# Optimization experiments

Hardware: AMD Instinct MI355X
Metric: run time of the kernel (lower is better)

## Reference

```python
import jax, jax.numpy as jnp
import numpy as np

N = 100000
E = 3200000
D = 128
H = 128
BN_EPS = 1e-5


def setup_inputs() -> dict:
    key = jax.random.key(0)
    ks = jax.random.split(key, 8)
    x = jax.random.normal(ks[0], (N, D), dtype=jnp.float32)
    edge_index = jax.random.randint(ks[1], (2, E), 0, N, dtype=jnp.int64)
    edge_attr = jax.random.normal(ks[2], (E, 1), dtype=jnp.float32)
    # MLP params (Linear stores weight [out,in]; we keep [in,out] for x @ W)
    W1 = jax.random.normal(ks[3], (D, H), dtype=jnp.float32) / np.sqrt(D)
    b1 = jnp.zeros((H,), dtype=jnp.float32)
    W2 = jax.random.normal(ks[4], (H, H), dtype=jnp.float32) / np.sqrt(H)
    b2 = jnp.zeros((H,), dtype=jnp.float32)
    gamma = jnp.ones((H,), dtype=jnp.float32)
    beta = jnp.zeros((H,), dtype=jnp.float32)
    return {"x": x, "edge_index": edge_index, "edge_attr": edge_attr,
            "W1": W1, "b1": b1, "W2": W2, "b2": b2,
            "gamma": gamma, "beta": beta}


def reference(x, edge_index, edge_attr, W1, b1, W2, b2, gamma, beta):
    src, dst = edge_index[0], edge_index[1]
    # GIN aggregation: (1 + eps) * x_i + sum_{j->i} x_j, eps = 0
    agg = jax.ops.segment_sum(x[src], dst, num_segments=N)  # [N, D]
    h = x + agg
    # 2-layer MLP
    h = jax.nn.relu(h @ W1 + b1)
    h = h @ W2 + b2
    # outer ReLU
    h = jax.nn.relu(h)
    # BatchNorm1d (training mode: batch stats, biased variance)
    mean = jnp.mean(h, axis=0)
    var = jnp.mean(jnp.square(h - mean), axis=0)
    h = (h - mean) * jax.lax.rsqrt(var + BN_EPS) * gamma + beta
    return h
```

## Files before the change

### kernel.cpp

```cpp
#include <hip/hip_runtime.h>

#define N_NODES 100000
#define DIM 128
#define NBUCK 391
#define CAP 12288
#define PT_TILE 8192
#define PT_THR 512

typedef unsigned int u32;
typedef unsigned short u16;
typedef __attribute__((ext_vector_type(8))) short bf16x8;
typedef __attribute__((ext_vector_type(4))) float f32x4;

__device__ __forceinline__ float bf16_to_f(u16 v) {
  return __uint_as_float(((u32)v) << 16);
}
__device__ __forceinline__ u16 f_to_bf16(float f) {
  u32 b = __float_as_uint(f);
  b += 0x7fff + ((b >> 16) & 1);
  return (u16)(b >> 16);
}
__device__ __forceinline__ float blo(u32 q) { return __uint_as_float(q << 16); }
__device__ __forceinline__ float bhi(u32 q) {
  return __uint_as_float(q & 0xffff0000u);
}
__device__ __forceinline__ u32 packbf(float lo, float hi) {
  return ((u32)f_to_bf16(hi) << 16) | (u32)f_to_bf16(lo);
}

__global__ __launch_bounds__(256) void prep_kernel(
    const float* __restrict__ W1, u16* __restrict__ Wt1,
    const float* __restrict__ W2, u16* __restrict__ Wt2,
    const int* __restrict__ ei, int* __restrict__ bcnt, int E_) {
  int blk = blockIdx.x;
  if (blk < 64) {
    int id = blk * 256 + threadIdx.x;
    Wt1[id] = f_to_bf16(W1[(id & 127) * DIM + (id >> 7)]);
  } else if (blk < 128) {
    int id = (blk - 64) * 256 + threadIdx.x;
    Wt2[id] = f_to_bf16(W2[(id & 127) * DIM + (id >> 7)]);
  } else {
    __shared__ int lc[NBUCK];
    for (int i = threadIdx.x; i < NBUCK; i += 256) lc[i] = 0;
    __syncthreads();
    const int* dst = ei + E_;
    int G = 512 * 256;
    int g = (blk - 128) * 256 + threadIdx.x;
    int n4 = E_ >> 2;
    const int4* d4 = (const int4*)dst;
    for (int i = g; i < n4; i += G) {
      int4 v = d4[i];
      atomicAdd(&lc[((u32)v.x) >> 8], 1);
      atomicAdd(&lc[((u32)v.y) >> 8], 1);
      atomicAdd(&lc[((u32)v.z) >> 8], 1);
      atomicAdd(&lc[((u32)v.w) >> 8], 1);
    }
    for (int e = (n4 << 2) + g; e < E_; e += G)
      atomicAdd(&lc[((u32)dst[e]) >> 8], 1);
    __syncthreads();
    for (int i = threadIdx.x; i < NBUCK; i += 256)
      if (lc[i]) atomicAdd(&bcnt[i], lc[i]);
  }
}

__global__ void bscan_kernel(const int* __restrict__ bcnt,
                             int* __restrict__ boffs, int* __restrict__ gcur) {
  __shared__ int s[256];
  int t = threadIdx.x;
  int v0 = (2 * t < NBUCK) ? bcnt[2 * t] : 0;
  int v1 = (2 * t + 1 < NBUCK) ? bcnt[2 * t + 1] : 0;
  int ts = v0 + v1;
  s[t] = ts;
  __syncthreads();
  for (int o = 1; o < 256; o <<= 1) {
    int u = (t >= o) ? s[t - o] : 0;
    __syncthreads();
    s[t] += u;
    __syncthreads();
  }
  int excl = s[t] - ts;
  if (2 * t <= NBUCK) boffs[2 * t] = excl;
  if (2 * t + 1 <= NBUCK) boffs[2 * t + 1] = excl + v0;
  if (2 * t < NBUCK) gcur[2 * t] = excl;
  if (2 * t + 1 < NBUCK) gcur[2 * t + 1] = excl + v0;
}

__global__ __launch_bounds__(PT_THR) void part_cvt_kernel(
    const int* __restrict__ ei, int* __restrict__ gcur,
    u32* __restrict__ packed, int E_, const float* __restrict__ x,
    u16* __restrict__ xb) {
  __shared__ u32 keys[PT_TILE];
  __shared__ u16 bid[PT_TILE];
  __shared__ int lh[NBUCK];
  __shared__ int lpos[NBUCK];
  __shared__ int gpos[NBUCK];
  __shared__ int ss[PT_THR];
  const int nPart = (E_ + PT_TILE - 1) / PT_TILE;
  const int t = threadIdx.x;

  if (blockIdx.x >= nPart) {
    int cb = blockIdx.x - nPart;
    int total = N_NODES * DIM / 4;
    int stride = 1024 * PT_THR;
    for (int i = cb * PT_THR + t; i < total; i += stride) {
      float4 v = reinterpret_cast<const float4*>(x)[i];
      ushort4 o;
      o.x = f_to_bf16(v.x);
      o.y = f_to_bf16(v.y);
      o.z = f_to_bf16(v.z);
      o.w = f_to_bf16(v.w);
      reinterpret_cast<ushort4*>(xb)[i] = o;
    }
    return;
  }

  const int base = blockIdx.x * PT_TILE;
  const int cnt = min(PT_TILE, E_ - base);

  for (int i = t; i < NBUCK; i += PT_THR) lh[i] = 0;
  __syncthreads();

  u32 pk[16];
  int bb[16];
#pragma unroll
  for (int k = 0; k < 16; ++k) {
    int e = base + k * PT_THR + t;
    if (k * PT_THR + t < cnt) {
      int src = ei[e];
      u32 dst = (u32)ei[E_ + e];
      bb[k] = (int)(dst >> 8);
      pk[k] = (u32)src | ((dst & 255u) << 17);
      atomicAdd(&lh[bb[k]], 1);
    } else {
      bb[k] = -1;
    }
  }
  __syncthreads();

  int v = (t < NBUCK) ? lh[t] : 0;
  ss[t] = v;
  __syncthreads();
  for (int o = 1; o < PT_THR; o <<= 1) {
    int u = (t >= o) ? ss[t - o] : 0;
    __syncthreads();
    ss[t] += u;
    __syncthreads();
  }
  if (t < NBUCK) {
    lpos[t] = ss[t] - v;
    if (v > 0) gpos[t] = atomicAdd(&gcur[t], v);
  }
  __syncthreads();

#pragma unroll
  for (int k = 0; k < 16; ++k) {
    if (bb[k] >= 0) {
      int p = atomicAdd(&lpos[bb[k]], 1);
      keys[p] = pk[k];
      bid[p] = (u16)bb[k];
    }
  }
  __syncthreads();

  for (int i = t; i < cnt; i += PT_THR) {
    int b = bid[i];
    int startb = lpos[b] - lh[b];
    packed[gpos[b] + (i - startb)] = keys[i];
  }
}

__global__ __launch_bounds__(256) void bsort_kernel(u32* __restrict__ packed,
                                                    const int* __restrict__ boffs,
                                                    int* __restrict__ offs,
                                                    int E_) {
  __shared__ u32 sorted_[CAP];
  __shared__ int hist[256], cur[256], ss[256];
  const int b = blockIdx.x, t = threadIdx.x;
  int base = boffs[b];
  int cnt = boffs[b + 1] - base;
  if (cnt > CAP) cnt = CAP;
  hist[t] = 0;
  __syncthreads();
  for (int i = t; i < cnt; i += 256) atomicAdd(&hist[packed[base + i] >> 17], 1);
  __syncthreads();
  int hv = hist[t];
  ss[t] = hv;
  __syncthreads();
  for (int o = 1; o < 256; o <<= 1) {
    int u = (t >= o) ? ss[t - o] : 0;
    __syncthreads();
    ss[t] += u;
    __syncthreads();
  }
  int excl = ss[t] - hv;
  cur[t] = excl;
  __syncthreads();
  for (int i = t; i < cnt; i += 256) {
    u32 v = packed[base + i];
    int p = atomicAdd(&cur[v >> 17], 1);
    sorted_[p] = v & 0x1FFFFu;
  }
  __syncthreads();
  for (int i = t; i < cnt; i += 256) packed[base + i] = sorted_[i];
  int node = b * 256 + t;
  if (node < N_NODES) offs[node] = base + excl;
  if (b == 0 && t == 0) offs[N_NODES] = E_;
}

__global__ __launch_bounds__(256) void gather_bf16_kernel(
    const uint4* __restrict__ xb4, const int* __restrict__ offs,
    const int* __restrict__ csr, uint4* __restrict__ hb4) {
  int n = blockIdx.x * 4 + (threadIdx.x >> 6);
  int lane = threadIdx.x & 63;
  int g = lane >> 4;
  int l = lane & 15;
  int beg = offs[n], end = offs[n + 1];
  float a0 = 0.f, a1 = 0.f, a2 = 0.f, a3 = 0.f;
  float a4 = 0.f, a5 = 0.f, a6 = 0.f, a7 = 0.f;
  if (g == 0) {
    uint4 q = xb4[(size_t)n * 16 + l];
    a0 = blo(q.x); a1 = bhi(q.x);
    a2 = blo(q.y); a3 = bhi(q.y);
    a4 = blo(q.z); a5 = bhi(q.z);
    a6 = blo(q.w); a7 = bhi(q.w);
  }
  int j = beg + g;
  for (; j + 12 < end; j += 16) {
    int s0 = csr[j], s1 = csr[j + 4], s2 = csr[j + 8], s3 = csr[j + 12];
    uint4 q0 = xb4[(size_t)s0 * 16 + l];
    uint4 q1 = xb4[(size_t)s1 * 16 + l];
    uint4 q2 = xb4[(size_t)s2 * 16 + l];
    uint4 q3 = xb4[(size_t)s3 * 16 + l];
    a0 += blo(q0.x); a1 += bhi(q0.x);
    a2 += blo(q0.y); a3 += bhi(q0.y);
    a4 += blo(q0.z); a5 += bhi(q0.z);
    a6 += blo(q0.w); a7 += bhi(q0.w);
    a0 += blo(q1.x); a1 += bhi(q1.x);
    a2 += blo(q1.y); a3 += bhi(q1.y);
    a4 += blo(q1.z); a5 += bhi(q1.z);
    a6 += blo(q1.w); a7 += bhi(q1.w);
    a0 += blo(q2.x); a1 += bhi(q2.x);
    a2 += blo(q2.y); a3 += bhi(q2.y);
    a4 += blo(q2.z); a5 += bhi(q2.z);
    a6 += blo(q2.w); a7 += bhi(q2.w);
    a0 += blo(q3.x); a1 += bhi(q3.x);
    a2 += blo(q3.y); a3 += bhi(q3.y);
    a4 += blo(q3.z); a5 += bhi(q3.z);
    a6 += blo(q3.w); a7 += bhi(q3.w);
  }
  for (; j < end; j += 4) {
    uint4 q = xb4[(size_t)csr[j] * 16 + l];
    a0 += blo(q.x); a1 += bhi(q.x);
    a2 += blo(q.y); a3 += bhi(q.y);
    a4 += blo(q.z); a5 += bhi(q.z);
    a6 += blo(q.w); a7 += bhi(q.w);
  }
  a0 += __shfl_xor(a0, 16); a1 += __shfl_xor(a1, 16);
  a2 += __shfl_xor(a2, 16); a3 += __shfl_xor(a3, 16);
  a4 += __shfl_xor(a4, 16); a5 += __shfl_xor(a5, 16);
  a6 += __shfl_xor(a6, 16); a7 += __shfl_xor(a7, 16);
  a0 += __shfl_xor(a0, 32); a1 += __shfl_xor(a1, 32);
  a2 += __shfl_xor(a2, 32); a3 += __shfl_xor(a3, 32);
  a4 += __shfl_xor(a4, 32); a5 += __shfl_xor(a5, 32);
  a6 += __shfl_xor(a6, 32); a7 += __shfl_xor(a7, 32);
  if (g == 0) {
    uint4 o;
    o.x = packbf(a0, a1);
    o.y = packbf(a2, a3);
    o.z = packbf(a4, a5);
    o.w = packbf(a6, a7);
    hb4[(size_t)n * 16 + l] = o;
  }
}

__global__ __launch_bounds__(256) void mlp_mfma_kernel(
    u16* __restrict__ hb, const u16* __restrict__ Wt1,
    const u16* __restrict__ Wt2, const float* __restrict__ b1,
    const float* __restrict__ b2, float* __restrict__ pstats) {
  __shared__ u16 sH1[4][16 * DIM];
  __shared__ float sS[4][128], sQ[4][128];
  const int tid = threadIdx.x;
  const int wv = tid >> 6;
  const int lane = tid & 63;
  const int lr = lane & 15;
  const int lq = lane >> 4;
  const int row0 = blockIdx.x * 64 + wv * 16;

  bf16x8 a[4];
  {
    int r = row0 + lr;
    if (r > N_NODES - 1) r = N_NODES - 1;
#pragma unroll
    for (int ks = 0; ks < 4; ++ks)
      a[ks] = *reinterpret_cast<const bf16x8*>(hb + (size_t)r * DIM + ks * 32 +
                                               lq * 8);
  }
  f32x4 acc[8];
#pragma unroll
  for (int ct = 0; ct < 8; ++ct) {
    f32x4 c = {0.f, 0.f, 0.f, 0.f};
#pragma unroll
    for (int ks = 0; ks < 4; ++ks) {
      bf16x8 b = *reinterpret_cast<const bf16x8*>(
          Wt1 + (ct * 16 + lr) * DIM + ks * 32 + lq * 8);
      c = __builtin_amdgcn_mfma_f32_16x16x32_bf16(a[ks], b, c, 0, 0, 0);
    }
    acc[ct] = c;
  }
  char* slab = reinterpret_cast<char*>(&sH1[wv][0]);
#pragma unroll
  for (int ct = 0; ct < 8; ++ct) {
    int c = ct * 16 + lr;
    float bias = b1[c];
#pragma unroll
    for (int j = 0; j < 4; ++j) {
      int rl = lq * 4 + j;
      float y = fmaxf(acc[ct][j] + bias, 0.f);
      int byte = rl * 256 + ((c * 2) ^ ((rl & 7) << 4));
      *reinterpret_cast<u16*>(slab + byte) = f_to_bf16(y);
    }
  }
  __syncthreads();

  bf16x8 a2[4];
#pragma unroll
  for (int ks = 0; ks < 4; ++ks) {
    int byte = lr * 256 + (((ks * 32 + lq * 8) * 2) ^ ((lr & 7) << 4));
    a2[ks] = *reinterpret_cast<const bf16x8*>(slab + byte);
  }
#pragma unroll
  for (int ct = 0; ct < 8; ++ct) {
    f32x4 c = {0.f, 0.f, 0.f, 0.f};
#pragma unroll
    for (int ks = 0; ks < 4; ++ks) {
      bf16x8 b = *reinterpret_cast<const bf16x8*>(
          Wt2 + (ct * 16 + lr) * DIM + ks * 32 + lq * 8);
      c = __builtin_amdgcn_mfma_f32_16x16x32_bf16(a2[ks], b, c, 0, 0, 0);
    }
    acc[ct] = c;
  }
  float ls[8], lss[8];
#pragma unroll
  for (int ct = 0; ct < 8; ++ct) {
    int c = ct * 16 + lr;
    float bias = b2[c];
    ls[ct] = 0.f;
    lss[ct] = 0.f;
#pragma unroll
    for (int j = 0; j < 4; ++j) {
      int r = row0 + lq * 4 + j;
      float y = fmaxf(acc[ct][j] + bias, 0.f);
      u16 yq = f_to_bf16(y);
      float yf = bf16_to_f(yq);
      if (r < N_NODES) {
        hb[(size_t)r * DIM + c] = yq;
        ls[ct] += yf;
        lss[ct] += yf * yf;
      }
    }
  }
#pragma unroll
  for (int ct = 0; ct < 8; ++ct) {
    float s = ls[ct], q = lss[ct];
    s += __shfl_xor(s, 16);
    q += __shfl_xor(q, 16);
    s += __shfl_xor(s, 32);
    q += __shfl_xor(q, 32);
    if (lq == 0) {
      sS[wv][ct * 16 + lr] = s;
      sQ[wv][ct * 16 + lr] = q;
    }
  }
  __syncthreads();
  {
    int t = tid;
    float v;
    if (t < 128)
      v = sS[0][t] + sS[1][t] + sS[2][t] + sS[3][t];
    else
      v = sQ[0][t - 128] + sQ[1][t - 128] + sQ[2][t - 128] + sQ[3][t - 128];
    pstats[(size_t)blockIdx.x * 256 + t] = v;
  }
}

__global__ __launch_bounds__(256) void bn_reduce_kernel(
    const float* __restrict__ pstats, float* __restrict__ stats, int nblk) {
  int t = threadIdx.x;
  float v = 0.f;
  for (int i = blockIdx.x; i < nblk; i += gridDim.x)
    v += pstats[(size_t)i * 256 + t];
  atomicAdd(&stats[t], v);
}

__global__ __launch_bounds__(256) void bn_apply_bf16_kernel(
    const uint4* __restrict__ hb4, const float* __restrict__ stats,
    const float* __restrict__ gamma, const float* __restrict__ beta,
    float4* __restrict__ out4) {
  __shared__ float sSc[128], sSh[128];
  int t = threadIdx.x;
  if (t < 128) {
    float mean = stats[t] / (float)N_NODES;
    float var = stats[128 + t] / (float)N_NODES - mean * mean;
    float scale = gamma[t] * rsqrtf(var + 1e-5f);
    sSc[t] = scale;
    sSh[t] = beta[t] - mean * scale;
  }
  __syncthreads();
  int total = N_NODES * 16;
  int stride = gridDim.x * 256;
  for (int i = blockIdx.x * 256 + t; i < total; i += stride) {
    uint4 q = hb4[i];
    int cb = (i & 15) * 8;
    float4 o0, o1;
    o0.x = blo(q.x) * sSc[cb + 0] + sSh[cb + 0];
    o0.y = bhi(q.x) * sSc[cb + 1] + sSh[cb + 1];
    o0.z = blo(q.y) * sSc[cb + 2] + sSh[cb + 2];
    o0.w = bhi(q.y) * sSc[cb + 3] + sSh[cb + 3];
    o1.x = blo(q.z) * sSc[cb + 4] + sSh[cb + 4];
    o1.y = bhi(q.z) * sSc[cb + 5] + sSh[cb + 5];
    o1.z = blo(q.w) * sSc[cb + 6] + sSh[cb + 6];
    o1.w = bhi(q.w) * sSc[cb + 7] + sSh[cb + 7];
    out4[2 * i] = o0;
    out4[2 * i + 1] = o1;
  }
}

__global__ __launch_bounds__(256) void hist_kernel(const int* __restrict__ ei,
                                                   int* __restrict__ deg,
                                                   int E_) {
  int stride = gridDim.x * blockDim.x;
  for (int e = blockIdx.x * blockDim.x + threadIdx.x; e < E_; e += stride)
    atomicAdd(&deg[ei[E_ + e]], 1);
}

__global__ __launch_bounds__(256) void scan_block_kernel(
    const int* __restrict__ deg, int* __restrict__ offs,
    int* __restrict__ partials, int n) {
  const int tid = threadIdx.x;
  int g = blockIdx.x * 1024 + tid * 4;
  int v0 = (g + 0 < n) ? deg[g + 0] : 0;
  int v1 = (g + 1 < n) ? deg[g + 1] : 0;
  int v2 = (g + 2 < n) ? deg[g + 2] : 0;
  int v3 = (g + 3 < n) ? deg[g + 3] : 0;
  int tsum = v0 + v1 + v2 + v3;
  __shared__ int s[256];
  s[tid] = tsum;
  __syncthreads();
  for (int off = 1; off < 256; off <<= 1) {
    int t = (tid >= off) ? s[tid - off] : 0;
    __syncthreads();
    s[tid] += t;
    __syncthreads();
  }
  int excl = s[tid] - tsum;
  if (g + 0 < n) offs[g + 0] = excl;
  if (g + 1 < n) offs[g + 1] = excl + v0;
  if (g + 2 < n) offs[g + 2] = excl + v0 + v1;
  if (g + 3 < n) offs[g + 3] = excl + v0 + v1 + v2;
  if (tid == 255) partials[blockIdx.x] = s[255];
}

__global__ void scan_partials_kernel(int* __restrict__ partials, int nb) {
  const int tid = threadIdx.x;
  int v = (tid < nb) ? partials[tid] : 0;
  __shared__ int s[128];
  s[tid] = v;
  __syncthreads();
  for (int off = 1; off < 128; off <<= 1) {
    int t = (tid >= off) ? s[tid - off] : 0;
    __syncthreads();
    s[tid] += t;
    __syncthreads();
  }
  if (tid < nb) partials[tid] = s[tid] - v;
}

__global__ __launch_bounds__(256) void scan_add_kernel(
    int* __restrict__ offs, int* __restrict__ cursor,
    const int* __restrict__ partials, int n, int E_) {
  int g = blockIdx.x * blockDim.x + threadIdx.x;
  if (g < n) {
    int v = offs[g] + partials[g >> 10];
    offs[g] = v;
    cursor[g] = v;
  }
  if (g == 0) offs[n] = E_;
}

__global__ __launch_bounds__(256) void fill_kernel(const int* __restrict__ ei,
                                                   int* __restrict__ cursor,
                                                   int* __restrict__ csr,
                                                   int E_) {
  const int G = gridDim.x * blockDim.x;
  int g = blockIdx.x * blockDim.x + threadIdx.x;
  for (long long base = g; base < E_; base += (long long)G * 8) {
    int src[8], dst[8], pos[8];
#pragma unroll
    for (int k = 0; k < 8; ++k) {
      long long e = base + (long long)k * G;
      src[k] = (e < E_) ? ei[e] : -1;
      dst[k] = (e < E_) ? ei[E_ + e] : 0;
    }
#pragma unroll
    for (int k = 0; k < 8; ++k)
      if (src[k] >= 0) pos[k] = atomicAdd(&cursor[dst[k]], 1);
#pragma unroll
    for (int k = 0; k < 8; ++k)
      if (src[k] >= 0) csr[pos[k]] = src[k];
  }
}

__global__ __launch_bounds__(128) void gather_f32_kernel(
    const float* __restrict__ x, const int* __restrict__ offs,
    const int* __restrict__ csr, float* __restrict__ h) {
  int n = blockIdx.x;
  int c = threadIdx.x;
  int beg = offs[n], end = offs[n + 1];
  float acc = x[(size_t)n * DIM + c];
  for (int j = beg; j < end; ++j) acc += x[(size_t)csr[j] * DIM + c];
  h[(size_t)n * DIM + c] = acc;
}

__global__ __launch_bounds__(256) void scatter_kernel(
    const float* __restrict__ x, const int* __restrict__ ei,
    float* __restrict__ h, int E_) {
  long long total = (long long)E_ * 32;
  long long stride = (long long)gridDim.x * blockDim.x;
  for (long long idx = (long long)blockIdx.x * blockDim.x + threadIdx.x;
       idx < total; idx += stride) {
    int e = (int)(idx >> 5);
    int q = (int)(idx & 31);
    float4 v =
        *reinterpret_cast<const float4*>(x + (size_t)ei[e] * DIM + q * 4);
    float* p = h + (size_t)ei[E_ + e] * DIM + q * 4;
    atomicAdd(p + 0, v.x);
    atomicAdd(p + 1, v.y);
    atomicAdd(p + 2, v.z);
    atomicAdd(p + 3, v.w);
  }
}

__global__ __launch_bounds__(256) void add_x_kernel(const float* __restrict__ x,
                                                    float* __restrict__ h) {
  size_t total = (size_t)N_NODES * DIM / 4;
  size_t stride = (size_t)gridDim.x * blockDim.x;
  for (size_t i = (size_t)blockIdx.x * blockDim.x + threadIdx.x; i < total;
       i += stride) {
    float4 v = reinterpret_cast<float4*>(h)[i];
    float4 xv = reinterpret_cast<const float4*>(x)[i];
    v.x += xv.x; v.y += xv.y; v.z += xv.z; v.w += xv.w;
    reinterpret_cast<float4*>(h)[i] = v;
  }
}

__global__ __launch_bounds__(256) void mlp_valu_kernel(
    float* hbuf, const float* __restrict__ W1, const float* __restrict__ b1,
    const float* __restrict__ W2, const float* __restrict__ b2) {
  __shared__ float sW[DIM * DIM];
  __shared__ float sH[32][DIM];
  const int tid = threadIdx.x;
  const int col = tid & 127;
  const int rhalf = tid >> 7;
  const int row0 = blockIdx.x * 32;

  for (int i = tid; i < DIM * DIM; i += 256) sW[i] = W1[i];
  for (int i = tid; i < 32 * DIM; i += 256) {
    int r = i >> 7, c = i & 127;
    sH[r][c] = hbuf[(size_t)(row0 + r) * DIM + c];
  }
  __syncthreads();
  float acc[16];
  float bias = b1[col];
#pragma unroll
  for (int j = 0; j < 16; ++j) acc[j] = bias;
#pragma unroll 4
  for (int k = 0; k < DIM; ++k) {
    float w = sW[k * DIM + col];
#pragma unroll
    for (int j = 0; j < 16; ++j) acc[j] = fmaf(sH[2 * j + rhalf][k], w, acc[j]);
  }
  __syncthreads();
  for (int i = tid; i < DIM * DIM; i += 256) sW[i] = W2[i];
#pragma unroll
  for (int j = 0; j < 16; ++j) sH[2 * j + rhalf][col] = fmaxf(acc[j], 0.f);
  __syncthreads();
  float bias2 = b2[col];
#pragma unroll
  for (int j = 0; j < 16; ++j) acc[j] = bias2;
#pragma unroll 4
  for (int k = 0; k < DIM; ++k) {
    float w = sW[k * DIM + col];
#pragma unroll
    for (int j = 0; j < 16; ++j) acc[j] = fmaf(sH[2 * j + rhalf][k], w, acc[j]);
  }
#pragma unroll
  for (int j = 0; j < 16; ++j)
    hbuf[(size_t)(row0 + 2 * j + rhalf) * DIM + col] = fmaxf(acc[j], 0.f);
}

__global__ __launch_bounds__(256) void bn_stats_kernel(
    const float* __restrict__ h, float* __restrict__ stats) {
  int col = threadIdx.x & 127;
  int rsub = threadIdx.x >> 7;
  int rstep = gridDim.x * 2;
  float s = 0.f, ss = 0.f;
  for (int r = blockIdx.x * 2 + rsub; r < N_NODES; r += rstep) {
    float v = h[(size_t)r * DIM + col];
    s += v;
    ss += v * v;
  }
  __shared__ float ls[256], lss[256];
  ls[threadIdx.x] = s;
  lss[threadIdx.x] = ss;
  __syncthreads();
  if (threadIdx.x < 128) {
    atomicAdd(&stats[col], ls[threadIdx.x] + ls[threadIdx.x + 128]);
    atomicAdd(&stats[DIM + col], lss[threadIdx.x] + lss[threadIdx.x + 128]);
  }
}

__global__ void bn_scale_kernel(const float* __restrict__ stats,
                                const float* __restrict__ gamma,
                                const float* __restrict__ beta,
                                float* __restrict__ sc) {
  int c = threadIdx.x;
  float mean = stats[c] / (float)N_NODES;
  float var = stats[DIM + c] / (float)N_NODES - mean * mean;
  float scale = gamma[c] * rsqrtf(var + 1e-5f);
  sc[c] = scale;
  sc[DIM + c] = beta[c] - mean * scale;
}

__global__ __launch_bounds__(256) void bn_apply_kernel(
    float* __restrict__ h, const float* __restrict__ sc) {
  size_t total = (size_t)N_NODES * DIM / 4;
  size_t stride = (size_t)gridDim.x * blockDim.x;
  for (size_t i = (size_t)blockIdx.x * blockDim.x + threadIdx.x; i < total;
       i += stride) {
    float4 v = reinterpret_cast<float4*>(h)[i];
    int c = (int)((i * 4) & 127);
    v.x = v.x * sc[c + 0] + sc[DIM + c + 0];
    v.y = v.y * sc[c + 1] + sc[DIM + c + 1];
    v.z = v.z * sc[c + 2] + sc[DIM + c + 2];
    v.w = v.w * sc[c + 3] + sc[DIM + c + 3];
    reinterpret_cast<float4*>(h)[i] = v;
  }
}

extern "C" void kernel_launch(void* const* d_in, const int* in_sizes, int n_in,
                              void* d_out, int out_size, void* d_ws,
                              size_t ws_size, hipStream_t stream) {
  const float* x = (const float*)d_in[0];
  const int* ei = (const int*)d_in[1];
  const float* W1 = (const float*)d_in[3];
  const float* b1 = (const float*)d_in[4];
  const float* W2 = (const float*)d_in[5];
  const float* b2 = (const float*)d_in[6];
  const float* gamma = (const float*)d_in[7];
  const float* beta = (const float*)d_in[8];
  float* out = (float*)d_out;
  int E_ = in_sizes[1] / 2;

  const size_t XB_B = (size_t)N_NODES * DIM * 2;
  char* w = (char*)d_ws;
  size_t off = 0;
  u16* xb = (u16*)(w + off); off += XB_B;
  u16* hb = (u16*)(w + off); off += XB_B;
  u16* Wt1 = (u16*)(w + off); off += 32768;
  u16* Wt2 = (u16*)(w + off); off += 32768;
  u32* packed = (u32*)(w + off); off += (size_t)E_ * 4;
  int* offs = (int*)(w + off); off += ((size_t)N_NODES + 4) * 4;
  int* bcnt = (int*)(w + off); off += 1600;
  float* stats = (float*)(w + off); off += 3072;
  int* boffs = (int*)(w + off); off += 1600;
  int* gcur = (int*)(w + off); off += 1600;
  size_t need_full = off;
  float* pstats = (float*)xb;

  int* f_offs = (int*)d_ws;
  int* f_cursor = f_offs + N_NODES + 1;
  int* f_partials = f_cursor + N_NODES;
  int* f_csr = f_partials + 128;
  float* f_stats = (float*)(f_csr + E_);
  size_t need_csr = ((size_t)2 * N_NODES + 129 + E_) * 4 + 3072;

  const int nScanBlocks = (N_NODES + 1023) / 1024;
  const int nEdgeBlocks = (E_ + 2047) / 2048;
  const int nPartBlocks = (E_ + PT_TILE - 1) / PT_TILE;
  const int nMlpBlocks = (N_NODES + 63) / 64;

  if (ws_size >= need_full) {
    hipMemsetAsync(bcnt, 0, 1600 + 3072, stream);
    prep_kernel<<<640, 256, 0, stream>>>(W1, Wt1, W2, Wt2, ei, bcnt, E_);
    bscan_kernel<<<1, 256, 0, stream>>>(bcnt, boffs, gcur);
    part_cvt_kernel<<<nPartBlocks + 1024, PT_THR, 0, stream>>>(
        ei, gcur, packed, E_, x, xb);
    bsort_kernel<<<NBUCK, 256, 0, stream>>>(packed, boffs, offs, E_);
    gather_bf16_kernel<<<N_NODES / 4, 256, 0, stream>>>(
        (const uint4*)xb, offs, (const int*)packed, (uint4*)hb);
    mlp_mfma_kernel<<<nMlpBlocks, 256, 0, stream>>>(hb, Wt1, Wt2, b1, b2,
                                                    pstats);
    bn_reduce_kernel<<<32, 256, 0, stream>>>(pstats, stats, nMlpBlocks);
    bn_apply_bf16_kernel<<<2048, 256, 0, stream>>>(
        (const uint4*)hb, stats, gamma, beta, (float4*)out);
  } else if (ws_size >= need_csr) {
    hipMemsetAsync(f_cursor, 0, (size_t)N_NODES * sizeof(int), stream);
    hipMemsetAsync(f_stats, 0, 768 * sizeof(float), stream);
    hist_kernel<<<2048, 256, 0, stream>>>(ei, f_cursor, E_);
    scan_block_kernel<<<nScanBlocks, 256, 0, stream>>>(f_cursor, f_offs,
                                                       f_partials, N_NODES);
    scan_partials_kernel<<<1, 128, 0, stream>>>(f_partials, nScanBlocks);
    scan_add_kernel<<<(N_NODES + 255) / 256, 256, 0, stream>>>(
        f_offs, f_cursor, f_partials, N_NODES, E_);
    fill_kernel<<<nEdgeBlocks, 256, 0, stream>>>(ei, f_cursor, f_csr, E_);
    gather_f32_kernel<<<N_NODES, 128, 0, stream>>>(x, f_offs, f_csr, out);
    mlp_valu_kernel<<<(N_NODES + 31) / 32, 256, 0, stream>>>(out, W1, b1, W2,
                                                             b2);
    bn_stats_kernel<<<1024, 256, 0, stream>>>(out, f_stats);
    bn_scale_kernel<<<1, 128, 0, stream>>>(f_stats, gamma, beta, f_stats + 256);
    bn_apply_kernel<<<2048, 256, 0, stream>>>(out, f_stats + 256);
  } else {
    float* s2 = (float*)d_ws;
    hipMemsetAsync(out, 0, (size_t)N_NODES * DIM * sizeof(float), stream);
    hipMemsetAsync(s2, 0, 768 * sizeof(float), stream);
    scatter_kernel<<<4096, 256, 0, stream>>>(x, ei, out, E_);
    add_x_kernel<<<2048, 256, 0, stream>>>(x, out);
    mlp_valu_kernel<<<(N_NODES + 31) / 32, 256, 0, stream>>>(out, W1, b1, W2,
                                                             b2);
    bn_stats_kernel<<<1024, 256, 0, stream>>>(out, s2);
    bn_scale_kernel<<<1, 128, 0, stream>>>(s2, gamma, beta, s2 + 256);
    bn_apply_kernel<<<2048, 256, 0, stream>>>(out, s2 + 256);
  }
}
```

Measured before the change: 276.4 us.

## Fuse bucket sort with neighbor gather using shared-memory sorted edge list

Merges the per-bucket counting sort and the bf16 gather-sum into one kernel with 1024-thread blocks. Sorted source indices and per-node offsets stay in LDS instead of being written back to global memory and re-read by a separate gather launch. This drops the global offs array and one kernel launch. In exchange the gather now runs on only 391 blocks of 16 waves, far fewer than the previous 25000 blocks, which may leave CUs underused and reduce latency hiding for the random row loads.

```diff
diff --git a/kernel.cpp b/kernel.cpp
--- a/kernel.cpp
+++ b/kernel.cpp
@@ -169,107 +169,113 @@
   }
 }
 
-__global__ __launch_bounds__(256) void bsort_kernel(u32* __restrict__ packed,
-                                                    const int* __restrict__ boffs,
-                                                    int* __restrict__ offs,
-                                                    int E_) {
+__global__ __launch_bounds__(1024) void sortgather_kernel(
+    const u32* __restrict__ packed, const int* __restrict__ boffs,
+    const uint4* __restrict__ xb4, uint4* __restrict__ hb4) {
   __shared__ u32 sorted_[CAP];
-  __shared__ int hist[256], cur[256], ss[256];
-  const int b = blockIdx.x, t = threadIdx.x;
+  __shared__ int hist[256], cur[256], ssc[256];
+  __shared__ int nodeoff[257];
+  const int b = blockIdx.x;
+  const int t = threadIdx.x;
   int base = boffs[b];
   int cnt = boffs[b + 1] - base;
   if (cnt > CAP) cnt = CAP;
-  hist[t] = 0;
-  __syncthreads();
-  for (int i = t; i < cnt; i += 256) atomicAdd(&hist[packed[base + i] >> 17], 1);
-  __syncthreads();
-  int hv = hist[t];
-  ss[t] = hv;
+
+  if (t < 256) hist[t] = 0;
+  __syncthreads();
+  for (int i = t; i < cnt; i += 1024)
+    atomicAdd(&hist[packed[base + i] >> 17], 1);
+  __syncthreads();
+  if (t < 256) ssc[t] = hist[t];
   __syncthreads();
   for (int o = 1; o < 256; o <<= 1) {
-    int u = (t >= o) ? ss[t - o] : 0;
-    __syncthreads();
-    ss[t] += u;
-    __syncthreads();
-  }
-  int excl = ss[t] - hv;
-  cur[t] = excl;
-  __syncthreads();
-  for (int i = t; i < cnt; i += 256) {
+    int u = 0;
+    if (t < 256 && t >= o) u = ssc[t - o];
+    __syncthreads();
+    if (t < 256) ssc[t] += u;
+    __syncthreads();
+  }
+  if (t < 256) {
+    int excl = ssc[t] - hist[t];
+    cur[t] = excl;
+    nodeoff[t] = excl;
+  }
+  if (t == 0) nodeoff[256] = cnt;
+  __syncthreads();
+  for (int i = t; i < cnt; i += 1024) {
     u32 v = packed[base + i];
     int p = atomicAdd(&cur[v >> 17], 1);
     sorted_[p] = v & 0x1FFFFu;
   }
   __syncthreads();
-  for (int i = t; i < cnt; i += 256) packed[base + i] = sorted_[i];
-  int node = b * 256 + t;
-  if (node < N_NODES) offs[node] = base + excl;
-  if (b == 0 && t == 0) offs[N_NODES] = E_;
-}
-
-__global__ __launch_bounds__(256) void gather_bf16_kernel(
-    const uint4* __restrict__ xb4, const int* __restrict__ offs,
-    const int* __restrict__ csr, uint4* __restrict__ hb4) {
-  int n = blockIdx.x * 4 + (threadIdx.x >> 6);
-  int lane = threadIdx.x & 63;
-  int g = lane >> 4;
-  int l = lane & 15;
-  int beg = offs[n], end = offs[n + 1];
-  float a0 = 0.f, a1 = 0.f, a2 = 0.f, a3 = 0.f;
-  float a4 = 0.f, a5 = 0.f, a6 = 0.f, a7 = 0.f;
-  if (g == 0) {
-    uint4 q = xb4[(size_t)n * 16 + l];
-    a0 = blo(q.x); a1 = bhi(q.x);
-    a2 = blo(q.y); a3 = bhi(q.y);
-    a4 = blo(q.z); a5 = bhi(q.z);
-    a6 = blo(q.w); a7 = bhi(q.w);
-  }
-  int j = beg + g;
-  for (; j + 12 < end; j += 16) {
-    int s0 = csr[j], s1 = csr[j + 4], s2 = csr[j + 8], s3 = csr[j + 12];
-    uint4 q0 = xb4[(size_t)s0 * 16 + l];
-    uint4 q1 = xb4[(size_t)s1 * 16 + l];
-    uint4 q2 = xb4[(size_t)s2 * 16 + l];
-    uint4 q3 = xb4[(size_t)s3 * 16 + l];
-    a0 += blo(q0.x); a1 += bhi(q0.x);
-    a2 += blo(q0.y); a3 += bhi(q0.y);
-    a4 += blo(q0.z); a5 += bhi(q0.z);
-    a6 += blo(q0.w); a7 += bhi(q0.w);
-    a0 += blo(q1.x); a1 += bhi(q1.x);
-    a2 += blo(q1.y); a3 += bhi(q1.y);
-    a4 += blo(q1.z); a5 += bhi(q1.z);
-    a6 += blo(q1.w); a7 += bhi(q1.w);
-    a0 += blo(q2.x); a1 += bhi(q2.x);
-    a2 += blo(q2.y); a3 += bhi(q2.y);
-    a4 += blo(q2.z); a5 += bhi(q2.z);
-    a6 += blo(q2.w); a7 += bhi(q2.w);
-    a0 += blo(q3.x); a1 += bhi(q3.x);
-    a2 += blo(q3.y); a3 += bhi(q3.y);
-    a4 += blo(q3.z); a5 += bhi(q3.z);
-    a6 += blo(q3.w); a7 += bhi(q3.w);
-  }
-  for (; j < end; j += 4) {
-    uint4 q = xb4[(size_t)csr[j] * 16 + l];
-    a0 += blo(q.x); a1 += bhi(q.x);
-    a2 += blo(q.y); a3 += bhi(q.y);
-    a4 += blo(q.z); a5 += bhi(q.z);
-    a6 += blo(q.w); a7 += bhi(q.w);
-  }
-  a0 += __shfl_xor(a0, 16); a1 += __shfl_xor(a1, 16);
-  a2 += __shfl_xor(a2, 16); a3 += __shfl_xor(a3, 16);
-  a4 += __shfl_xor(a4, 16); a5 += __shfl_xor(a5, 16);
-  a6 += __shfl_xor(a6, 16); a7 += __shfl_xor(a7, 16);
-  a0 += __shfl_xor(a0, 32); a1 += __shfl_xor(a1, 32);
-  a2 += __shfl_xor(a2, 32); a3 += __shfl_xor(a3, 32);
-  a4 += __shfl_xor(a4, 32); a5 += __shfl_xor(a5, 32);
-  a6 += __shfl_xor(a6, 32); a7 += __shfl_xor(a7, 32);
-  if (g == 0) {
-    uint4 o;
-    o.x = packbf(a0, a1);
-    o.y = packbf(a2, a3);
-    o.z = packbf(a4, a5);
-    o.w = packbf(a6, a7);
-    hb4[(size_t)n * 16 + l] = o;
+
+  const int wv = t >> 6;
+  const int lane = t & 63;
+  const int g = lane >> 4;
+  const int l = lane & 15;
+#pragma unroll 1
+  for (int k = 0; k < 16; ++k) {
+    int nl = wv + (k << 4);
+    int n = b * 256 + nl;
+    if (n >= N_NODES) break;
+    int beg = nodeoff[nl], end = nodeoff[nl + 1];
+    float a0 = 0.f, a1 = 0.f, a2 = 0.f, a3 = 0.f;
+    float a4 = 0.f, a5 = 0.f, a6 = 0.f, a7 = 0.f;
+    if (g == 0) {
+      uint4 q = xb4[(size_t)n * 16 + l];
+      a0 = blo(q.x); a1 = bhi(q.x);
+      a2 = blo(q.y); a3 = bhi(q.y);
+      a4 = blo(q.z); a5 = bhi(q.z);
+      a6 = blo(q.w); a7 = bhi(q.w);
+    }
+    int j = beg + g;
+    for (; j + 12 < end; j += 16) {
+      int s0 = sorted_[j], s1 = sorted_[j + 4];
+      int s2 = sorted_[j + 8], s3 = sorted_[j + 12];
+      uint4 q0 = xb4[(size_t)s0 * 16 + l];
+      uint4 q1 = xb4[(size_t)s1 * 16 + l];
+      uint4 q2 = xb4[(size_t)s2 * 16 + l];
+      uint4 q3 = xb4[(size_t)s3 * 16 + l];
+      a0 += blo(q0.x); a1 += bhi(q0.x);
+      a2 += blo(q0.y); a3 += bhi(q0.y);
+      a4 += blo(q0.z); a5 += bhi(q0.z);
+      a6 += blo(q0.w); a7 += bhi(q0.w);
+      a0 += blo(q1.x); a1 += bhi(q1.x);
+      a2 += blo(q1.y); a3 += bhi(q1.y);
+      a4 += blo(q1.z); a5 += bhi(q1.z);
+      a6 += blo(q1.w); a7 += bhi(q1.w);
+      a0 += blo(q2.x); a1 += bhi(q2.x);
+      a2 += blo(q2.y); a3 += bhi(q2.y);
+      a4 += blo(q2.z); a5 += bhi(q2.z);
+      a6 += blo(q2.w); a7 += bhi(q2.w);
+      a0 += blo(q3.x); a1 += bhi(q3.x);
+      a2 += blo(q3.y); a3 += bhi(q3.y);
+      a4 += blo(q3.z); a5 += bhi(q3.z);
+      a6 += blo(q3.w); a7 += bhi(q3.w);
+    }
+    for (; j < end; j += 4) {
+      uint4 q = xb4[(size_t)sorted_[j] * 16 + l];
+      a0 += blo(q.x); a1 += bhi(q.x);
+      a2 += blo(q.y); a3 += bhi(q.y);
+      a4 += blo(q.z); a5 += bhi(q.z);
+      a6 += blo(q.w); a7 += bhi(q.w);
+    }
+    a0 += __shfl_xor(a0, 16); a1 += __shfl_xor(a1, 16);
+    a2 += __shfl_xor(a2, 16); a3 += __shfl_xor(a3, 16);
+    a4 += __shfl_xor(a4, 16); a5 += __shfl_xor(a5, 16);
+    a6 += __shfl_xor(a6, 16); a7 += __shfl_xor(a7, 16);
+    a0 += __shfl_xor(a0, 32); a1 += __shfl_xor(a1, 32);
+    a2 += __shfl_xor(a2, 32); a3 += __shfl_xor(a3, 32);
+    a4 += __shfl_xor(a4, 32); a5 += __shfl_xor(a5, 32);
+    a6 += __shfl_xor(a6, 32); a7 += __shfl_xor(a7, 32);
+    if (g == 0) {
+      uint4 o;
+      o.x = packbf(a0, a1);
+      o.y = packbf(a2, a3);
+      o.z = packbf(a4, a5);
+      o.w = packbf(a6, a7);
+      hb4[(size_t)n * 16 + l] = o;
+    }
   }
 }
 
@@ -669,7 +675,6 @@
   u16* Wt1 = (u16*)(w + off); off += 32768;
   u16* Wt2 = (u16*)(w + off); off += 32768;
   u32* packed = (u32*)(w + off); off += (size_t)E_ * 4;
-  int* offs = (int*)(w + off); off += ((size_t)N_NODES + 4) * 4;
   int* bcnt = (int*)(w + off); off += 1600;
   float* stats = (float*)(w + off); off += 3072;
   int* boffs = (int*)(w + off); off += 1600;
@@ -695,9 +700,8 @@
     bscan_kernel<<<1, 256, 0, stream>>>(bcnt, boffs, gcur);
     part_cvt_kernel<<<nPartBlocks + 1024, PT_THR, 0, stream>>>(
         ei, gcur, packed, E_, x, xb);
-    bsort_kernel<<<NBUCK, 256, 0, stream>>>(packed, boffs, offs, E_);
-    gather_bf16_kernel<<<N_NODES / 4, 256, 0, stream>>>(
-        (const uint4*)xb, offs, (const int*)packed, (uint4*)hb);
+    sortgather_kernel<<<NBUCK, 1024, 0, stream>>>(
+        packed, boffs, (const uint4*)xb, (uint4*)hb);
     mlp_mfma_kernel<<<nMlpBlocks, 256, 0, stream>>>(hb, Wt1, Wt2, b1, b2,
                                                     pstats);
     bn_reduce_kernel<<<32, 256, 0, stream>>>(pstats, stats, nMlpBlocks);
```

After: 259.5 us. 1.06x faster.
